# Performance work log

Hardware: AMD Instinct MI355X
Metric: run time of the kernel (lower is better)

Reference implementation:

```python
import jax, jax.numpy as jnp
import numpy as np
import math

FACTOR = 5  # ProbAttention factor default


def setup_inputs() -> dict:
    key = jax.random.key(0)
    k1, k2, k3, k4 = jax.random.split(key, 4)
    B, L, S, H, D = 4, 2048, 2048, 8, 64
    sample_k = min(FACTOR * math.ceil(math.log(L)), S)  # = 40
    return {
        "queries": jax.random.normal(k1, (B, L, H, D), dtype=jnp.float32),
        "keys": jax.random.normal(k2, (B, S, H, D), dtype=jnp.float32),
        "values": jax.random.normal(k3, (B, S, H, D), dtype=jnp.float32),
        # torch.randint(0, L_keys, (L_queries, sample_k)) hoisted out for determinism
        "index_sample": jax.random.randint(k4, (L, sample_k), 0, S, dtype=jnp.int32),
    }


def reference(queries, keys, values, index_sample):
    B, L, H, D = queries.shape
    S = keys.shape[1]
    # [B, H, L, D] layout as in forward's transpose(1, 2)
    q = jnp.transpose(queries, (0, 2, 1, 3))
    k = jnp.transpose(keys, (0, 2, 1, 3))
    v = jnp.transpose(values, (0, 2, 1, 3))

    n_top = min(FACTOR * math.ceil(math.log(S)) if S > 1 else 1, L)
    scale = 1.0 / math.sqrt(D)

    # --- _prob_QK ---
    # sampled keys per query position: [B, H, L, u, D]
    k_samp = k[:, :, index_sample, :]
    qk_sample = jnp.einsum('bhld,bhlud->bhlu', q, k_samp)  # [B, H, L, u]
    # sparsity measure M = max - mean (sum divided by full key length S)
    M = qk_sample.max(axis=-1) - qk_sample.sum(axis=-1) / S  # [B, H, L]
    M_top = jax.lax.top_k(M, n_top)[1]  # [B, H, n_top] query indices
    q_red = jnp.take_along_axis(q, M_top[..., None], axis=2)  # [B, H, n_top, D]
    scores = jnp.einsum('bhnd,bhsd->bhns', q_red, k) * scale  # [B, H, n_top, S]

    # --- softmax over keys (dropout p=0 -> identity) ---
    attn = jax.nn.softmax(scores, axis=-1)

    # --- initial context = mean of V, then scatter-update selected queries ---
    ctx_top = jnp.einsum('bhns,bhsd->bhnd', attn, v)  # [B, H, n_top, D]
    context = jnp.broadcast_to(v.mean(axis=2, keepdims=True), (B, H, L, D))
    bi = jnp.arange(B)[:, None, None]
    hi = jnp.arange(H)[None, :, None]
    context = context.at[bi, hi, M_top].set(ctx_top)

    return jnp.transpose(context, (0, 2, 1, 3))  # [B, L, H, D]
```

## Files before the change

kernel.cpp:

```cpp
#include <hip/hip_runtime.h>
#include <math.h>

constexpr int B = 4, L = 2048, S = 2048, H = 8, D = 64;
constexpr int U  = 40;
constexpr int NT = 40;
constexpr float SCALE = 0.125f;

__global__ void k_compute_M(const float* __restrict__ q, const float* __restrict__ k,
                            const int* __restrict__ idx, float* __restrict__ M) {
    int tid = threadIdx.x;
    int wid = tid >> 6, lane = tid & 63;
    int b = blockIdx.x & 3;
    int l = (blockIdx.x >> 2) * 4 + wid;
    int h = lane >> 3, dg = lane & 7;

    const float4* qr = (const float4*)(q + ((size_t)(b * L + l) * H + h) * D + dg * 8);
    float4 q0 = qr[0], q1 = qr[1];

    const int* irow = idx + l * U;
    const float* kb = k + (size_t)b * S * H * D + (size_t)h * D + dg * 8;
    float vmax = -INFINITY, vsum = 0.f;
#pragma unroll 4
    for (int u = 0; u < U; u++) {
        int s = irow[u];
        const float4* kr = (const float4*)(kb + (size_t)s * H * D);
        float4 k0 = kr[0], k1 = kr[1];
        float acc = q0.x * k0.x + q0.y * k0.y + q0.z * k0.z + q0.w * k0.w
                  + q1.x * k1.x + q1.y * k1.y + q1.z * k1.z + q1.w * k1.w;
        acc += __shfl_xor(acc, 1);
        acc += __shfl_xor(acc, 2);
        acc += __shfl_xor(acc, 4);
        vmax = fmaxf(vmax, acc);
        vsum += acc;
    }
    if (dg == 0) M[(size_t)(b * H + h) * L + l] = vmax - vsum / (float)S;
}

__device__ inline unsigned int fkey(float f) {
    unsigned int u = __float_as_uint(f);
    return (u & 0x80000000u) ? ~u : (u | 0x80000000u);
}

__global__ void k_topk(const float* __restrict__ M, int* __restrict__ topidx) {
    int bh = blockIdx.x;
    const float* m = M + (size_t)bh * L;
    int tid = threadIdx.x;

    __shared__ int hist[256];
    __shared__ unsigned int prefix_s;
    __shared__ int c_above_s, nsel_s, ntie_s, r_s;
    __shared__ int tie_i[L];

    unsigned int o[8];
    const float4* mr = (const float4*)(m + tid * 8);
    float4 a0 = mr[0], a1 = mr[1];
    o[0] = fkey(a0.x); o[1] = fkey(a0.y); o[2] = fkey(a0.z); o[3] = fkey(a0.w);
    o[4] = fkey(a1.x); o[5] = fkey(a1.y); o[6] = fkey(a1.z); o[7] = fkey(a1.w);

    if (tid == 0) { prefix_s = 0u; c_above_s = 0; nsel_s = 0; ntie_s = 0; }

    for (int sh = 24; sh >= 0; sh -= 8) {
        hist[tid] = 0;
        __syncthreads();
        unsigned int pfx = prefix_s;
#pragma unroll
        for (int j = 0; j < 8; j++) {
            bool match = (sh == 24) || ((o[j] >> (sh + 8)) == (pfx >> (sh + 8)));
            if (match) atomicAdd(&hist[(o[j] >> sh) & 0xFF], 1);
        }
        __syncthreads();
        if (tid < 64) {
            int4 hv = *(const int4*)&hist[tid * 4];
            int lsum = hv.x + hv.y + hv.z + hv.w;
            int s = lsum;
#pragma unroll
            for (int off = 1; off < 64; off <<= 1) {
                int t = __shfl_down(s, off);
                if (tid + off < 64) s += t;
            }
            int tail = s - lsum;
            int acc = c_above_s;
            int need = NT - acc;
            int t3 = tail + hv.w;
            int t2 = t3 + hv.z;
            int t1 = t2 + hv.y;
            int t0 = t1 + hv.x;
            if (t0 >= need && t1 < need) { prefix_s |= (unsigned)(4 * tid + 0) << sh; c_above_s = acc + t1; }
            else if (t1 >= need && t2 < need) { prefix_s |= (unsigned)(4 * tid + 1) << sh; c_above_s = acc + t2; }
            else if (t2 >= need && t3 < need) { prefix_s |= (unsigned)(4 * tid + 2) << sh; c_above_s = acc + t3; }
            else if (t3 >= need && tail < need) { prefix_s |= (unsigned)(4 * tid + 3) << sh; c_above_s = acc + tail; }
        }
        __syncthreads();
    }

    unsigned int T = prefix_s;

#pragma unroll
    for (int j = 0; j < 8; j++) {
        if (o[j] > T) {
            int slot = atomicAdd(&nsel_s, 1);
            topidx[bh * NT + slot] = tid * 8 + j;
        } else if (o[j] == T) {
            int p = atomicAdd(&ntie_s, 1);
            tie_i[p] = tid * 8 + j;
        }
    }
    __syncthreads();
    if (tid == 0) r_s = NT - nsel_s;
    __syncthreads();
    int r = r_s, ntie = ntie_s;

#pragma unroll
    for (int j = 0; j < 8; j++) {
        if (o[j] == T) {
            int myidx = tid * 8 + j;
            int rank = 0;
            for (int p = 0; p < ntie; p++) rank += (tie_i[p] < myidx) ? 1 : 0;
            if (rank < r) {
                int slot = atomicAdd(&nsel_s, 1);
                topidx[bh * NT + slot] = myidx;
            }
        }
    }
}

__global__ void k_meanv_part(const float* __restrict__ v, float* __restrict__ part) {
    int blk = blockIdx.x;
    int b = blk >> 5, c = blk & 31;
    int col = threadIdx.x;
    const float* p = v + ((size_t)(b * S + c * 64)) * 512 + col;
    float acc = 0.f;
#pragma unroll
    for (int s = 0; s < 64; s++) acc += p[(size_t)s * 512];
    part[(size_t)blk * 512 + col] = acc;
}

__global__ void k_meanv_final(const float* __restrict__ part, float* __restrict__ meanv) {
    int b = blockIdx.x; int col = threadIdx.x;
    float acc = 0.f;
#pragma unroll
    for (int c = 0; c < 32; c++) acc += part[(size_t)(b * 32 + c) * 512 + col];
    meanv[b * 512 + col] = acc * (1.f / (float)S);
}

template <int NCH_>
__global__ __launch_bounds__(512) void k_attn_part(
        const float* __restrict__ q, const float* __restrict__ k,
        const float* __restrict__ v, const int* __restrict__ topidx,
        float* __restrict__ pctx, float* __restrict__ pm, float* __restrict__ pl) {
    constexpr int CS_ = S / NCH_;
    constexpr int CPL = CS_ / 128;
    int blk = blockIdx.x;
    int bh = blk / NCH_, c = blk % NCH_;
    int b = bh / H, h = bh % H;
    int s0 = c * CS_;
    int tid = threadIdx.x;
    int lane = tid & 63, g = tid >> 6;

    __shared__ float q_s[NT][D];
    __shared__ float p_s[NT][CS_ + 4];
    __shared__ float m_c[NT];

    for (int i = tid; i < NT * D; i += 512) {
        int n = i >> 6, d = i & 63;
        int lsel = topidx[bh * NT + n];
        q_s[n][d] = q[((size_t)(b * L + lsel) * H + h) * D + d];
    }
    __syncthreads();

    int rg = g & 3, ch = g >> 2;
    int r0 = rg * 10;
    int lc = ch * (CS_ / 2) + lane * CPL;
    const float* kp = k + ((size_t)(b * S + s0 + lc) * H + h) * D;

    float sc[10][CPL];
#pragma unroll
    for (int j = 0; j < 10; j++)
#pragma unroll
        for (int p = 0; p < CPL; p++) sc[j][p] = 0.f;

#pragma unroll
    for (int dc = 0; dc < 64; dc += 16) {
        float4 kf[CPL][4];
#pragma unroll
        for (int p = 0; p < CPL; p++) {
            const float* kc = kp + (size_t)p * H * D + dc;
            kf[p][0] = *(const float4*)(kc);
            kf[p][1] = *(const float4*)(kc + 4);
            kf[p][2] = *(const float4*)(kc + 8);
            kf[p][3] = *(const float4*)(kc + 12);
        }
#pragma unroll
        for (int j = 0; j < 10; j++) {
            const float4* qr = (const float4*)&q_s[r0 + j][dc];
            float4 q0 = qr[0], q1 = qr[1], q2 = qr[2], q3 = qr[3];
#pragma unroll
            for (int p = 0; p < CPL; p++) {
                sc[j][p] += q0.x * kf[p][0].x + q0.y * kf[p][0].y + q0.z * kf[p][0].z + q0.w * kf[p][0].w
                          + q1.x * kf[p][1].x + q1.y * kf[p][1].y + q1.z * kf[p][1].z + q1.w * kf[p][1].w
                          + q2.x * kf[p][2].x + q2.y * kf[p][2].y + q2.z * kf[p][2].z + q2.w * kf[p][2].w
                          + q3.x * kf[p][3].x + q3.y * kf[p][3].y + q3.z * kf[p][3].z + q3.w * kf[p][3].w;
            }
        }
    }
#pragma unroll
    for (int j = 0; j < 10; j++) {
#pragma unroll
        for (int p = 0; p < CPL; p++) sc[j][p] *= SCALE;
        if (CPL == 1) p_s[r0 + j][lc] = sc[j][0];
        else *(float2*)&p_s[r0 + j][lc] = make_float2(sc[j][0], sc[j][1]);
    }
    __syncthreads();

    for (int n = g; n < NT; n += 8) {
        float mx = -INFINITY;
#pragma unroll
        for (int jj = 0; jj < CS_ / 64; jj++) mx = fmaxf(mx, p_s[n][lane + 64 * jj]);
#pragma unroll
        for (int off = 1; off < 64; off <<= 1)
            mx = fmaxf(mx, __shfl_xor(mx, off));
        if (lane == 0) m_c[n] = mx;
    }
    __syncthreads();

#pragma unroll
    for (int j = 0; j < 10; j++) {
        float mm = m_c[r0 + j];
        if (CPL == 1) p_s[r0 + j][lc] = __expf(sc[j][0] - mm);
        else *(float2*)&p_s[r0 + j][lc] =
                 make_float2(__expf(sc[j][0] - mm), __expf(sc[j][1] - mm));
    }
    __syncthreads();

    for (int n = g; n < NT; n += 8) {
        float sum = 0.f;
#pragma unroll
        for (int jj = 0; jj < CS_ / 64; jj++) sum += p_s[n][lane + 64 * jj];
#pragma unroll
        for (int off = 1; off < 64; off <<= 1) sum += __shfl_xor(sum, off);
        if (lane == 0) {
            pm[(bh * NCH_ + c) * NT + n] = m_c[n];
            pl[(bh * NCH_ + c) * NT + n] = sum;
        }
    }

    float acc[5];
#pragma unroll
    for (int r = 0; r < 5; r++) acc[r] = 0.f;
    int rp = g * 5;
    const float* vb = v + ((size_t)(b * S + s0) * H + h) * D + lane;
    for (int t4 = 0; t4 < CS_; t4 += 4) {
        float vd0 = vb[(size_t)(t4 + 0) * H * D];
        float vd1 = vb[(size_t)(t4 + 1) * H * D];
        float vd2 = vb[(size_t)(t4 + 2) * H * D];
        float vd3 = vb[(size_t)(t4 + 3) * H * D];
#pragma unroll
        for (int r = 0; r < 5; r++) {
            float4 p4 = *(const float4*)&p_s[rp + r][t4];
            acc[r] += p4.x * vd0 + p4.y * vd1 + p4.z * vd2 + p4.w * vd3;
        }
    }
#pragma unroll
    for (int r = 0; r < 5; r++)
        pctx[((size_t)(bh * NCH_ + c) * NT + rp + r) * D + lane] = acc[r];
}

__global__ void k_fill(const float* __restrict__ meanv, float4* __restrict__ out) {
    int i = blockIdx.x * blockDim.x + threadIdx.x;
    int b = i >> 18;
    int col4 = i & 127;
    out[i] = ((const float4*)meanv)[(b << 7) | col4];
}

template <int NCH_>
__global__ void k_combine(const int* __restrict__ topidx, const float* __restrict__ pctx,
                          const float* __restrict__ pm, const float* __restrict__ pl,
                          float* __restrict__ out) {
    int bh = blockIdx.x; int b = bh / H, h = bh % H;
    int tid = threadIdx.x;
    for (int i = tid; i < NT * D; i += 256) {
        int n = i / D, d = i % D;
        float mg = -INFINITY;
#pragma unroll
        for (int c = 0; c < NCH_; c++) mg = fmaxf(mg, pm[(bh * NCH_ + c) * NT + n]);
        float lsum = 0.f, ctx = 0.f;
#pragma unroll
        for (int c = 0; c < NCH_; c++) {
            float w = __expf(pm[(bh * NCH_ + c) * NT + n] - mg);
            lsum += pl[(bh * NCH_ + c) * NT + n] * w;
            ctx  += pctx[((size_t)(bh * NCH_ + c) * NT + n) * D + d] * w;
        }
        int lsel = topidx[bh * NT + n];
        out[((size_t)(b * L + lsel) * H + h) * D + d] = ctx / lsum;
    }
}

extern "C" void kernel_launch(void* const* d_in, const int* in_sizes, int n_in,
                              void* d_out, int out_size, void* d_ws, size_t ws_size,
                              hipStream_t stream) {
    const float* q   = (const float*)d_in[0];
    const float* k   = (const float*)d_in[1];
    const float* v   = (const float*)d_in[2];
    const int*   idx = (const int*)d_in[3];
    float* out = (float*)d_out;

    float* ws = (float*)d_ws;
    float* M      = ws;
    int*   topidx = (int*)(ws + 65536);
    float* meanv  = ws + 65536 + 1280;
    float* pm     = meanv + 2048;

    k_compute_M<<<B * L / 4, 256, 0, stream>>>(q, k, idx, M);
    k_topk<<<B * H, 256, 0, stream>>>(M, topidx);
    k_meanv_part<<<B * 32, 512, 0, stream>>>(v, M);
    k_meanv_final<<<B, 512, 0, stream>>>(M, meanv);

    constexpr size_t base_floats = 65536 + 1280 + 2048;
    constexpr size_t need16 = (base_floats + 2ull * (32 * 16 * 40) + 32ull * 16 * 40 * 64) * 4;
    if (ws_size >= need16) {
        constexpr int NCH_ = 16;
        float* pl   = pm + 32 * NCH_ * NT;
        float* pctx = pl + 32 * NCH_ * NT;
        k_attn_part<NCH_><<<B * H * NCH_, 512, 0, stream>>>(q, k, v, topidx, pctx, pm, pl);
        k_fill<<<(B * L * H * D / 4) / 256, 256, 0, stream>>>(meanv, (float4*)out);
        k_combine<NCH_><<<B * H, 256, 0, stream>>>(topidx, pctx, pm, pl, out);
    } else {
        constexpr int NCH_ = 8;
        float* pl   = pm + 32 * NCH_ * NT;
        float* pctx = pl + 32 * NCH_ * NT;
        k_attn_part<NCH_><<<B * H * NCH_, 512, 0, stream>>>(q, k, v, topidx, pctx, pm, pl);
        k_fill<<<(B * L * H * D / 4) / 256, 256, 0, stream>>>(meanv, (float4*)out);
        k_combine<NCH_><<<B * H, 256, 0, stream>>>(topidx, pctx, pm, pl, out);
    }
}
```

Measured before the change: 171.0 us.

## Fuse mean-V reduction into M and top-k kernels, fold fill into attention

The mean-of-V partial sums now run as extra blocks of the M-computation kernel, and the final mean-V reduction runs as extra blocks of the top-k kernel. The output fill is folded into the tail of the attention-partial kernel. This cuts the launch count from seven to four and lets independent work share a launch, at the cost of a larger workspace and some load imbalance between block types.

New measurement: 162.0 us. -5.2%, faster.

```diff
diff --git a/kernel.cpp b/kernel.cpp
--- a/kernel.cpp
+++ b/kernel.cpp
@@ -6,34 +6,49 @@
 constexpr int NT = 40;
 constexpr float SCALE = 0.125f;
 
-__global__ void k_compute_M(const float* __restrict__ q, const float* __restrict__ k,
-                            const int* __restrict__ idx, float* __restrict__ M) {
+__global__ void k_M_meanvpart(const float* __restrict__ q, const float* __restrict__ k,
+                              const float* __restrict__ v, const int* __restrict__ idx,
+                              float* __restrict__ M, float* __restrict__ part) {
     int tid = threadIdx.x;
-    int wid = tid >> 6, lane = tid & 63;
-    int b = blockIdx.x & 3;
-    int l = (blockIdx.x >> 2) * 4 + wid;
-    int h = lane >> 3, dg = lane & 7;
-
-    const float4* qr = (const float4*)(q + ((size_t)(b * L + l) * H + h) * D + dg * 8);
-    float4 q0 = qr[0], q1 = qr[1];
-
-    const int* irow = idx + l * U;
-    const float* kb = k + (size_t)b * S * H * D + (size_t)h * D + dg * 8;
-    float vmax = -INFINITY, vsum = 0.f;
+    if (blockIdx.x < 2048) {
+        int wid = tid >> 6, lane = tid & 63;
+        int b = blockIdx.x & 3;
+        int l = (blockIdx.x >> 2) * 4 + wid;
+        int h = lane >> 3, dg = lane & 7;
+
+        const float4* qr = (const float4*)(q + ((size_t)(b * L + l) * H + h) * D + dg * 8);
+        float4 q0 = qr[0], q1 = qr[1];
+
+        const int* irow = idx + l * U;
+        const float* kb = k + (size_t)b * S * H * D + (size_t)h * D + dg * 8;
+        float vmax = -INFINITY, vsum = 0.f;
 #pragma unroll 4
-    for (int u = 0; u < U; u++) {
-        int s = irow[u];
-        const float4* kr = (const float4*)(kb + (size_t)s * H * D);
-        float4 k0 = kr[0], k1 = kr[1];
-        float acc = q0.x * k0.x + q0.y * k0.y + q0.z * k0.z + q0.w * k0.w
-                  + q1.x * k1.x + q1.y * k1.y + q1.z * k1.z + q1.w * k1.w;
-        acc += __shfl_xor(acc, 1);
-        acc += __shfl_xor(acc, 2);
-        acc += __shfl_xor(acc, 4);
-        vmax = fmaxf(vmax, acc);
-        vsum += acc;
-    }
-    if (dg == 0) M[(size_t)(b * H + h) * L + l] = vmax - vsum / (float)S;
+        for (int u = 0; u < U; u++) {
+            int s = irow[u];
+            const float4* kr = (const float4*)(kb + (size_t)s * H * D);
+            float4 k0 = kr[0], k1 = kr[1];
+            float acc = q0.x * k0.x + q0.y * k0.y + q0.z * k0.z + q0.w * k0.w
+                      + q1.x * k1.x + q1.y * k1.y + q1.z * k1.z + q1.w * k1.w;
+            acc += __shfl_xor(acc, 1);
+            acc += __shfl_xor(acc, 2);
+            acc += __shfl_xor(acc, 4);
+            vmax = fmaxf(vmax, acc);
+            vsum += acc;
+        }
+        if (dg == 0) M[(size_t)(b * H + h) * L + l] = vmax - vsum / (float)S;
+    } else {
+        int blk = blockIdx.x - 2048;
+        int b = blk >> 5, c = blk & 31;
+        const float* p = v + ((size_t)(b * S + c * 64)) * 512;
+        float a0 = 0.f, a1 = 0.f;
+#pragma unroll
+        for (int s = 0; s < 64; s++) {
+            a0 += p[(size_t)s * 512 + tid];
+            a1 += p[(size_t)s * 512 + tid + 256];
+        }
+        part[(size_t)blk * 512 + tid]       = a0;
+        part[(size_t)blk * 512 + tid + 256] = a1;
+    }
 }
 
 __device__ inline unsigned int fkey(float f) {
@@ -41,10 +56,23 @@
     return (u & 0x80000000u) ? ~u : (u | 0x80000000u);
 }
 
-__global__ void k_topk(const float* __restrict__ M, int* __restrict__ topidx) {
+__global__ void k_topk_meanv(const float* __restrict__ M, int* __restrict__ topidx,
+                             const float* __restrict__ part, float* __restrict__ meanv) {
+    int tid = threadIdx.x;
+    if (blockIdx.x >= 32) {
+        int b = blockIdx.x - 32;
+        float a0 = 0.f, a1 = 0.f;
+#pragma unroll
+        for (int c = 0; c < 32; c++) {
+            a0 += part[(size_t)(b * 32 + c) * 512 + tid];
+            a1 += part[(size_t)(b * 32 + c) * 512 + tid + 256];
+        }
+        meanv[b * 512 + tid]       = a0 * (1.f / (float)S);
+        meanv[b * 512 + tid + 256] = a1 * (1.f / (float)S);
+        return;
+    }
     int bh = blockIdx.x;
     const float* m = M + (size_t)bh * L;
-    int tid = threadIdx.x;
 
     __shared__ int hist[256];
     __shared__ unsigned int prefix_s;
@@ -124,30 +152,13 @@
     }
 }
 
-__global__ void k_meanv_part(const float* __restrict__ v, float* __restrict__ part) {
-    int blk = blockIdx.x;
-    int b = blk >> 5, c = blk & 31;
-    int col = threadIdx.x;
-    const float* p = v + ((size_t)(b * S + c * 64)) * 512 + col;
-    float acc = 0.f;
-#pragma unroll
-    for (int s = 0; s < 64; s++) acc += p[(size_t)s * 512];
-    part[(size_t)blk * 512 + col] = acc;
-}
-
-__global__ void k_meanv_final(const float* __restrict__ part, float* __restrict__ meanv) {
-    int b = blockIdx.x; int col = threadIdx.x;
-    float acc = 0.f;
-#pragma unroll
-    for (int c = 0; c < 32; c++) acc += part[(size_t)(b * 32 + c) * 512 + col];
-    meanv[b * 512 + col] = acc * (1.f / (float)S);
-}
-
 template <int NCH_>
-__global__ __launch_bounds__(512) void k_attn_part(
+__global__ __launch_bounds__(512) void k_attn_fill(
         const float* __restrict__ q, const float* __restrict__ k,
         const float* __restrict__ v, const int* __restrict__ topidx,
-        float* __restrict__ pctx, float* __restrict__ pm, float* __restrict__ pl) {
+        const float* __restrict__ meanv,
+        float* __restrict__ pctx, float* __restrict__ pm, float* __restrict__ pl,
+        float4* __restrict__ out4) {
     constexpr int CS_ = S / NCH_;
     constexpr int CPL = CS_ / 128;
     int blk = blockIdx.x;
@@ -263,13 +274,17 @@
 #pragma unroll
     for (int r = 0; r < 5; r++)
         pctx[((size_t)(bh * NCH_ + c) * NT + rp + r) * D + lane] = acc[r];
-}
-
-__global__ void k_fill(const float* __restrict__ meanv, float4* __restrict__ out) {
-    int i = blockIdx.x * blockDim.x + threadIdx.x;
-    int b = i >> 18;
-    int col4 = i & 127;
-    out[i] = ((const float4*)meanv)[(b << 7) | col4];
+
+    constexpr int FPB = 1048576 / (32 * NCH_);
+    const float4* mv4 = (const float4*)meanv;
+    size_t base = (size_t)blk * FPB;
+#pragma unroll
+    for (int j = 0; j < FPB / 512; j++) {
+        size_t i = base + tid + (size_t)j * 512;
+        int bb = (int)(i >> 18);
+        int col4 = (int)(i & 127);
+        out4[i] = mv4[(bb << 7) | col4];
+    }
 }
 
 template <int NCH_>
@@ -308,28 +323,27 @@
     float* M      = ws;
     int*   topidx = (int*)(ws + 65536);
     float* meanv  = ws + 65536 + 1280;
-    float* pm     = meanv + 2048;
-
-    k_compute_M<<<B * L / 4, 256, 0, stream>>>(q, k, idx, M);
-    k_topk<<<B * H, 256, 0, stream>>>(M, topidx);
-    k_meanv_part<<<B * 32, 512, 0, stream>>>(v, M);
-    k_meanv_final<<<B, 512, 0, stream>>>(M, meanv);
-
-    constexpr size_t base_floats = 65536 + 1280 + 2048;
+    float* part   = meanv + 2048;
+    float* pm     = part + 65536;
+
+    k_M_meanvpart<<<2048 + 128, 256, 0, stream>>>(q, k, v, idx, M, part);
+    k_topk_meanv<<<36, 256, 0, stream>>>(M, topidx, part, meanv);
+
+    constexpr size_t base_floats = 65536 + 1280 + 2048 + 65536;
     constexpr size_t need16 = (base_floats + 2ull * (32 * 16 * 40) + 32ull * 16 * 40 * 64) * 4;
     if (ws_size >= need16) {
         constexpr int NCH_ = 16;
         float* pl   = pm + 32 * NCH_ * NT;
         float* pctx = pl + 32 * NCH_ * NT;
-        k_attn_part<NCH_><<<B * H * NCH_, 512, 0, stream>>>(q, k, v, topidx, pctx, pm, pl);
-        k_fill<<<(B * L * H * D / 4) / 256, 256, 0, stream>>>(meanv, (float4*)out);
+        k_attn_fill<NCH_><<<B * H * NCH_, 512, 0, stream>>>(q, k, v, topidx, meanv,
+                                                            pctx, pm, pl, (float4*)out);
         k_combine<NCH_><<<B * H, 256, 0, stream>>>(topidx, pctx, pm, pl, out);
     } else {
         constexpr int NCH_ = 8;
         float* pl   = pm + 32 * NCH_ * NT;
         float* pctx = pl + 32 * NCH_ * NT;
-        k_attn_part<NCH_><<<B * H * NCH_, 512, 0, stream>>>(q, k, v, topidx, pctx, pm, pl);
-        k_fill<<<(B * L * H * D / 4) / 256, 256, 0, stream>>>(meanv, (float4*)out);
+        k_attn_fill<NCH_><<<B * H * NCH_, 512, 0, stream>>>(q, k, v, topidx, meanv,
+                                                            pctx, pm, pl, (float4*)out);
         k_combine<NCH_><<<B * H, 256, 0, stream>>>(topidx, pctx, pm, pl, out);
     }
 }
```
